# Kernel optimization log

Hardware: AMD Instinct MI355X
Metric: run time of the kernel (lower is better)

Reference implementation:

```python
import jax, jax.numpy as jnp
import numpy as np


def _knn_idx(pts, k):
    # pts: [N, d] -> indices of k nearest neighbors (incl. self, loop=True) [N, k]
    sq = jnp.sum(pts * pts, axis=-1)
    d2 = sq[:, None] + sq[None, :] - 2.0 * (pts @ pts.T)  # [N, N] squared dists
    _, idx = jax.lax.top_k(-d2, k)  # k smallest distances
    return idx


def _graph_conv(x, nbr, Wr, br, Ws):
    # x: [B, N, d_in], nbr: [B, N, k]. GraphConv (aggr='add'):
    # out_i = W_rel @ sum_j x_j + b_rel + W_root @ x_i
    gathered = jax.vmap(lambda xb, ib: xb[ib])(x, nbr)  # [B, N, k, d_in]
    agg = gathered.sum(axis=2)                          # [B, N, d_in]
    return agg @ Wr.T + br + x @ Ws.T


def setup_inputs() -> dict:
    key = jax.random.key(0)
    ks = jax.random.split(key, 10)
    B, N, D, H = 16, 2048, 3, 128
    s = lambda fi, fo: (2.0 / (fi + fo)) ** 0.5
    return {
        "point_cloud": jax.random.normal(ks[0], (B, N, D), dtype=jnp.float32),
        "W1r": jax.random.normal(ks[1], (H, D), dtype=jnp.float32) * s(D, H),
        "b1": jnp.zeros((H,), dtype=jnp.float32),
        "W1s": jax.random.normal(ks[2], (H, D), dtype=jnp.float32) * s(D, H),
        "W2r": jax.random.normal(ks[3], (H, H), dtype=jnp.float32) * s(H, H),
        "b2": jnp.zeros((H,), dtype=jnp.float32),
        "W2s": jax.random.normal(ks[4], (H, H), dtype=jnp.float32) * s(H, H),
        "W3r": jax.random.normal(ks[5], (H, H), dtype=jnp.float32) * s(H, H),
        "b3": jnp.zeros((H,), dtype=jnp.float32),
        "W3s": jax.random.normal(ks[6], (H, H), dtype=jnp.float32) * s(H, H),
        "k": 16,
    }


def reference(point_cloud, W1r, b1, W1s, W2r, b2, W2s, W3r, b3, W3s, k):
    # knn graph per batch element (loop=True: self-loop included, d(i,i)=0)
    nbr = jax.vmap(lambda p: _knn_idx(p, k))(point_cloud)  # [B, N, k]
    x = jax.nn.relu(_graph_conv(point_cloud, nbr, W1r, b1, W1s))
    x = jax.nn.relu(_graph_conv(x, nbr, W2r, b2, W2s))
    x = _graph_conv(x, nbr, W3r, b3, W3s)
    return x  # [B, N, output_dim]
```

## Files before the change

kernel.cpp:

```cpp
#include <hip/hip_runtime.h>
#include <math.h>

#define NPTS 2048
#define BATCH 16
#define KNN 16
#define HID 128
#define RPB 8
#define CAP 128

typedef __attribute__((ext_vector_type(8))) short bf16x8;
typedef __attribute__((ext_vector_type(4))) float f32x4;

__device__ inline unsigned short f2bf(float f) {
    unsigned u = __float_as_uint(f);
    return (unsigned short)((u + 0x7FFFu + ((u >> 16) & 1u)) >> 16);
}
__device__ inline float bflo(unsigned v) { return __uint_as_float(v << 16); }
__device__ inline float bfhi(unsigned v) { return __uint_as_float(v & 0xFFFF0000u); }

__global__ __launch_bounds__(512) void knn_kernel(
    const float* __restrict__ pc, int* __restrict__ nbr,
    const float* __restrict__ W1r, const float* __restrict__ b1,
    const float* __restrict__ W1s, unsigned short* __restrict__ x1)
{
    __shared__ __align__(16) float4 pts[NPTS];
    __shared__ unsigned ckey[RPB][CAP];
    __shared__ unsigned cidx[RPB][CAP];

    const int b = blockIdx.x >> 8;
    const int rblk = blockIdx.x & 255;
    const float* p = pc + (size_t)b * NPTS * 3;

    for (int t = threadIdx.x; t < NPTS; t += 512) {
        float x = p[t * 3 + 0], y = p[t * 3 + 1], z = p[t * 3 + 2];
        pts[t] = make_float4(x, y, z, x * x + y * y + z * z);
    }
    __syncthreads();

    const int w = threadIdx.x >> 6;
    const int lane = threadIdx.x & 63;
    const int i = rblk * RPB + w;
    const float4 pi = pts[i];
    const float piw16 = pi.w + 16.0f;

    unsigned key[32];
    unsigned km = 0xFFFFFFFFu;
    #pragma unroll
    for (int t = 0; t < 32; ++t) {
        float4 c = pts[t * 64 + lane];
        float dot = fmaf(pi.x, c.x, fmaf(pi.y, c.y, pi.z * c.z));
        float d2 = fmaf(-2.0f, dot, piw16 + c.w);
        key[t] = __float_as_uint(d2);
        km = min(km, key[t]);
    }

    unsigned v = km;
    #pragma unroll
    for (int k = 2; k <= 64; k <<= 1) {
        #pragma unroll
        for (int j = k >> 1; j > 0; j >>= 1) {
            unsigned o = (unsigned)__shfl_xor((int)v, j, 64);
            bool sel = ((lane & k) == 0) == ((lane & j) == 0);
            v = sel ? min(v, o) : max(v, o);
        }
    }
    const unsigned T0 = (unsigned)__shfl((int)v, 15, 64);

    unsigned base = 0;
    #pragma unroll 1
    for (int t = 0; t < 32; ++t) {
        bool pred = key[t] <= T0;
        unsigned long long mask = __ballot(pred);
        if (mask) {
            unsigned prefix = __builtin_amdgcn_mbcnt_hi(
                (unsigned)(mask >> 32),
                __builtin_amdgcn_mbcnt_lo((unsigned)mask, 0));
            unsigned pos = base + prefix;
            if (pred && pos < CAP) {
                ckey[w][pos] = key[t];
                cidx[w][pos] = (unsigned)(t * 64 + lane);
            }
            base += (unsigned)__popcll(mask);
        }
    }
    __threadfence_block();
    const int m = (int)base;

    int* out = nbr + ((size_t)b * NPTS + i) * KNN;
    float ax = 0.f, ay = 0.f, az = 0.f;

    if (m <= CAP) {
        unsigned k0 = (lane < m) ? ckey[w][lane] : 0xFFFFFFFFu;
        unsigned k1 = (lane + 64 < m) ? ckey[w][lane + 64] : 0xFFFFFFFFu;
        int r0 = 0, r1 = 0;
        if (m <= 64) {
            #pragma unroll 1
            for (int jj = 0; jj < m; ++jj) {
                unsigned kj = ckey[w][jj];
                r0 += (kj < k0) || (kj == k0 && jj < lane);
            }
        } else {
            #pragma unroll 1
            for (int jj = 0; jj < m; ++jj) {
                unsigned kj = ckey[w][jj];
                r0 += (kj < k0) || (kj == k0 && jj < lane);
                r1 += (kj < k1) || (kj == k1 && jj < lane + 64);
            }
        }
        if (lane < m && r0 < KNN) {
            unsigned j = cidx[w][lane];
            out[r0] = (int)j;
            float4 q = pts[j]; ax += q.x; ay += q.y; az += q.z;
        }
        if (m > 64 && lane + 64 < m && r1 < KNN) {
            unsigned j = cidx[w][lane + 64];
            out[r1] = (int)j;
            float4 q = pts[j]; ax += q.x; ay += q.y; az += q.z;
        }
    } else {
        unsigned T = 0;
        #pragma unroll 1
        for (int bit = 31; bit >= 0; --bit) {
            unsigned trial = T | (1u << bit);
            int cnt = 0;
            #pragma unroll
            for (int t = 0; t < 32; ++t) cnt += (key[t] < trial);
            #pragma unroll
            for (int off = 32; off; off >>= 1)
                cnt += __shfl_xor(cnt, off, 64);
            if (cnt < KNN) T = trial;
        }
        unsigned bs = 0;
        #pragma unroll 1
        for (int t = 0; t < 32; ++t) {
            bool p1 = key[t] < T;
            unsigned long long mask = __ballot(p1);
            if (mask) {
                unsigned prefix = __builtin_amdgcn_mbcnt_hi(
                    (unsigned)(mask >> 32),
                    __builtin_amdgcn_mbcnt_lo((unsigned)mask, 0));
                if (p1) {
                    out[bs + prefix] = t * 64 + lane;
                    float4 q = pts[t * 64 + lane];
                    ax += q.x; ay += q.y; az += q.z;
                }
                bs += (unsigned)__popcll(mask);
            }
        }
        #pragma unroll 1
        for (int t = 0; t < 32 && bs < KNN; ++t) {
            bool p2 = key[t] == T;
            unsigned long long mask = __ballot(p2);
            if (mask) {
                unsigned prefix = __builtin_amdgcn_mbcnt_hi(
                    (unsigned)(mask >> 32),
                    __builtin_amdgcn_mbcnt_lo((unsigned)mask, 0));
                unsigned pos = bs + prefix;
                if (p2 && pos < KNN) {
                    out[pos] = t * 64 + lane;
                    float4 q = pts[t * 64 + lane];
                    ax += q.x; ay += q.y; az += q.z;
                }
                bs += (unsigned)__popcll(mask);
            }
        }
    }

    #pragma unroll
    for (int off = 32; off; off >>= 1) {
        ax += __shfl_xor(ax, off, 64);
        ay += __shfl_xor(ay, off, 64);
        az += __shfl_xor(az, off, 64);
    }

    unsigned short* xrow = x1 + ((size_t)b * NPTS + i) * HID;
    #pragma unroll
    for (int hh = 0; hh < 2; ++hh) {
        int h = lane + hh * 64;
        float acc = b1[h];
        acc += W1r[h * 3 + 0] * ax + W1r[h * 3 + 1] * ay + W1r[h * 3 + 2] * az;
        acc += W1s[h * 3 + 0] * pi.x + W1s[h * 3 + 1] * pi.y + W1s[h * 3 + 2] * pi.z;
        xrow[h] = f2bf(fmaxf(acc, 0.f));
    }
}

__global__ __launch_bounds__(256) void wcvt_kernel(
    const float* __restrict__ a, const float* __restrict__ b,
    const float* __restrict__ c, const float* __restrict__ d,
    unsigned short* __restrict__ out)
{
    int g = blockIdx.x * 256 + threadIdx.x;
    int m = g >> 14;
    const float* s = (m == 0) ? a : (m == 1) ? b : (m == 2) ? c : d;
    out[g] = f2bf(s[g & 16383]);
}

template <bool RELU, bool OUT_BF16>
__global__ __launch_bounds__(512) void conv_fused(
    const unsigned short* __restrict__ x, const int* __restrict__ nbr,
    const unsigned short* __restrict__ Wr, const unsigned short* __restrict__ Ws,
    const float* __restrict__ bias, void* __restrict__ outv)
{
    __shared__ __align__(16) char smem[64 * 132 * 4];
    __shared__ int nbrs[64][17];
    unsigned short (*aggs)[136] = (unsigned short (*)[136])smem;
    float (*outs)[132] = (float (*)[132])smem;

    const int p0 = blockIdx.x * 64;
    const int bt = p0 >> 11;
    const unsigned short* xb = x + ((size_t)bt << 11) * HID;

    for (int e = threadIdx.x; e < 64 * KNN; e += 512)
        nbrs[e >> 4][e & 15] = nbr[(size_t)p0 * KNN + e];
    __syncthreads();

    #pragma unroll
    for (int it = 0; it < 2; ++it) {
        int task = it * 512 + threadIdx.x;
        int c8 = task & 15, pt = task >> 4;
        const unsigned short* base = xb + c8 * 8;
        float s[8] = {0, 0, 0, 0, 0, 0, 0, 0};
        #pragma unroll
        for (int t = 0; t < KNN; ++t) {
            int j = nbrs[pt][t];
            uint4 v = *(const uint4*)(base + (size_t)j * HID);
            s[0] += bflo(v.x); s[1] += bfhi(v.x);
            s[2] += bflo(v.y); s[3] += bfhi(v.y);
            s[4] += bflo(v.z); s[5] += bfhi(v.z);
            s[6] += bflo(v.w); s[7] += bfhi(v.w);
        }
        uint4 ov;
        ov.x = (unsigned)f2bf(s[0]) | ((unsigned)f2bf(s[1]) << 16);
        ov.y = (unsigned)f2bf(s[2]) | ((unsigned)f2bf(s[3]) << 16);
        ov.z = (unsigned)f2bf(s[4]) | ((unsigned)f2bf(s[5]) << 16);
        ov.w = (unsigned)f2bf(s[6]) | ((unsigned)f2bf(s[7]) << 16);
        *(uint4*)&aggs[pt][c8 * 8] = ov;
    }
    __syncthreads();

    const int wv = threadIdx.x >> 6;
    const int lane = threadIdx.x & 63;
    const int ptw = (wv & 1) * 32;
    const int h0w = (wv >> 1) * 32;
    const int row = lane & 15;
    const int quad = lane >> 4;

    f32x4 acc[2][2];
    #pragma unroll
    for (int i = 0; i < 2; ++i)
        #pragma unroll
        for (int n = 0; n < 2; ++n) acc[i][n] = (f32x4){0, 0, 0, 0};

    #pragma unroll
    for (int kc = 0; kc < 4; ++kc) {
        bf16x8 a0 = *(const bf16x8*)&aggs[ptw + row][quad * 8 + kc * 32];
        bf16x8 a1 = *(const bf16x8*)&aggs[ptw + 16 + row][quad * 8 + kc * 32];
        #pragma unroll
        for (int n = 0; n < 2; ++n) {
            bf16x8 bb = *(const bf16x8*)&Wr[(size_t)(h0w + n * 16 + row) * HID
                                            + quad * 8 + kc * 32];
            acc[0][n] = __builtin_amdgcn_mfma_f32_16x16x32_bf16(a0, bb, acc[0][n], 0, 0, 0);
            acc[1][n] = __builtin_amdgcn_mfma_f32_16x16x32_bf16(a1, bb, acc[1][n], 0, 0, 0);
        }
    }
    const unsigned short* xr0 = x + (size_t)(p0 + ptw + row) * HID + quad * 8;
    const unsigned short* xr1 = xr0 + 16 * HID;
    #pragma unroll
    for (int kc = 0; kc < 4; ++kc) {
        bf16x8 a0 = *(const bf16x8*)(xr0 + kc * 32);
        bf16x8 a1 = *(const bf16x8*)(xr1 + kc * 32);
        #pragma unroll
        for (int n = 0; n < 2; ++n) {
            bf16x8 bb = *(const bf16x8*)&Ws[(size_t)(h0w + n * 16 + row) * HID
                                            + quad * 8 + kc * 32];
            acc[0][n] = __builtin_amdgcn_mfma_f32_16x16x32_bf16(a0, bb, acc[0][n], 0, 0, 0);
            acc[1][n] = __builtin_amdgcn_mfma_f32_16x16x32_bf16(a1, bb, acc[1][n], 0, 0, 0);
        }
    }

    __syncthreads();
    #pragma unroll
    for (int n = 0; n < 2; ++n) {
        float bh = bias[h0w + n * 16 + row];
        #pragma unroll
        for (int i = 0; i < 2; ++i) {
            #pragma unroll
            for (int r = 0; r < 4; ++r) {
                int pt = ptw + i * 16 + quad * 4 + r;
                int hh = h0w + n * 16 + row;
                float vv = acc[i][n][r] + bh;
                if (RELU) vv = fmaxf(vv, 0.f);
                if (OUT_BF16) aggs[pt][hh] = f2bf(vv);
                else          outs[pt][hh] = vv;
            }
        }
    }
    __syncthreads();

    if (OUT_BF16) {
        unsigned short* o = (unsigned short*)outv;
        #pragma unroll
        for (int q = 0; q < 2; ++q) {
            int task = q * 512 + threadIdx.x;
            int rr = task >> 4, ch = task & 15;
            *(uint4*)(o + (size_t)(p0 + rr) * HID + ch * 8) =
                *(const uint4*)&aggs[rr][ch * 8];
        }
    } else {
        float* o = (float*)outv;
        #pragma unroll
        for (int q = 0; q < 4; ++q) {
            int task = q * 512 + threadIdx.x;
            int rr = task >> 5, ch = task & 31;
            *(float4*)(o + (size_t)(p0 + rr) * HID + ch * 4) =
                *(const float4*)&outs[rr][ch * 4];
        }
    }
}

extern "C" void kernel_launch(void* const* d_in, const int* in_sizes, int n_in,
                              void* d_out, int out_size, void* d_ws, size_t ws_size,
                              hipStream_t stream)
{
    const float* pc  = (const float*)d_in[0];
    const float* W1r = (const float*)d_in[1];
    const float* b1  = (const float*)d_in[2];
    const float* W1s = (const float*)d_in[3];
    const float* W2r = (const float*)d_in[4];
    const float* b2  = (const float*)d_in[5];
    const float* W2s = (const float*)d_in[6];
    const float* W3r = (const float*)d_in[7];
    const float* b3  = (const float*)d_in[8];
    const float* W3s = (const float*)d_in[9];
    float* out = (float*)d_out;

    char* ws = (char*)d_ws;
    const size_t MB = 1024 * 1024;
    int*            nbr = (int*)ws;
    unsigned short* x1  = (unsigned short*)(ws + 2 * MB);
    unsigned short* x2  = (unsigned short*)(ws + 2 * MB + 8388608);
    unsigned short* wbf = (unsigned short*)(ws + 2 * MB + 2 * 8388608);
    unsigned short* w2r = wbf;
    unsigned short* w2s = wbf + 16384;
    unsigned short* w3r = wbf + 32768;
    unsigned short* w3s = wbf + 49152;

    const int NPOINTS = BATCH * NPTS;

    wcvt_kernel<<<256, 256, 0, stream>>>(W2r, W2s, W3r, W3s, wbf);
    knn_kernel<<<NPOINTS / RPB, 512, 0, stream>>>(pc, nbr, W1r, b1, W1s, x1);

    conv_fused<true, true><<<NPOINTS / 64, 512, 0, stream>>>(
        x1, nbr, w2r, w2s, b2, x2);
    conv_fused<false, false><<<NPOINTS / 64, 512, 0, stream>>>(
        x2, nbr, w3r, w3s, b3, out);
}
```

Baseline: 174.4 us.

## Shrink conv tiles to 16 points, interleave batches across blocks, batch gather loads

The fused graph-conv kernel now processes 16 points per 256-thread block instead of 64 points per 512 threads. Block indices are interleaved across batch elements so concurrently running blocks touch different batches. The neighbor gather issues eight 16-byte loads before accumulating them, which raises memory-level parallelism. Smaller tiles give four times more blocks and less shared memory each, but every block re-reads the full Wr/Ws weight tiles, so weight traffic per point goes up.

```diff
diff --git a/kernel.cpp b/kernel.cpp
--- a/kernel.cpp
+++ b/kernel.cpp
@@ -196,38 +196,43 @@
 }
 
 template <bool RELU, bool OUT_BF16>
-__global__ __launch_bounds__(512) void conv_fused(
+__global__ __launch_bounds__(256) void conv_fused(
     const unsigned short* __restrict__ x, const int* __restrict__ nbr,
     const unsigned short* __restrict__ Wr, const unsigned short* __restrict__ Ws,
     const float* __restrict__ bias, void* __restrict__ outv)
 {
-    __shared__ __align__(16) char smem[64 * 132 * 4];
-    __shared__ int nbrs[64][17];
+    __shared__ __align__(16) char smem[16 * 132 * 4];
+    __shared__ int nbrs[16][17];
     unsigned short (*aggs)[136] = (unsigned short (*)[136])smem;
     float (*outs)[132] = (float (*)[132])smem;
 
-    const int p0 = blockIdx.x * 64;
-    const int bt = p0 >> 11;
+    const int bt = blockIdx.x & 15;
+    const int p0 = bt * NPTS + (blockIdx.x >> 4) * 16;
     const unsigned short* xb = x + ((size_t)bt << 11) * HID;
 
-    for (int e = threadIdx.x; e < 64 * KNN; e += 512)
-        nbrs[e >> 4][e & 15] = nbr[(size_t)p0 * KNN + e];
-    __syncthreads();
-
-    #pragma unroll
-    for (int it = 0; it < 2; ++it) {
-        int task = it * 512 + threadIdx.x;
-        int c8 = task & 15, pt = task >> 4;
+    nbrs[threadIdx.x >> 4][threadIdx.x & 15] =
+        nbr[(size_t)p0 * KNN + threadIdx.x];
+    __syncthreads();
+
+    {
+        const int c8 = threadIdx.x & 15, pt = threadIdx.x >> 4;
         const unsigned short* base = xb + c8 * 8;
         float s[8] = {0, 0, 0, 0, 0, 0, 0, 0};
         #pragma unroll
-        for (int t = 0; t < KNN; ++t) {
-            int j = nbrs[pt][t];
-            uint4 v = *(const uint4*)(base + (size_t)j * HID);
-            s[0] += bflo(v.x); s[1] += bfhi(v.x);
-            s[2] += bflo(v.y); s[3] += bfhi(v.y);
-            s[4] += bflo(v.z); s[5] += bfhi(v.z);
-            s[6] += bflo(v.w); s[7] += bfhi(v.w);
+        for (int half = 0; half < 2; ++half) {
+            uint4 v[8];
+            #pragma unroll
+            for (int t = 0; t < 8; ++t) {
+                int j = nbrs[pt][half * 8 + t];
+                v[t] = *(const uint4*)(base + (size_t)j * HID);
+            }
+            #pragma unroll
+            for (int t = 0; t < 8; ++t) {
+                s[0] += bflo(v[t].x); s[1] += bfhi(v[t].x);
+                s[2] += bflo(v[t].y); s[3] += bfhi(v[t].y);
+                s[4] += bflo(v[t].z); s[5] += bfhi(v[t].z);
+                s[6] += bflo(v[t].w); s[7] += bfhi(v[t].w);
+            }
         }
         uint4 ov;
         ov.x = (unsigned)f2bf(s[0]) | ((unsigned)f2bf(s[1]) << 16);
@@ -240,41 +245,33 @@
 
     const int wv = threadIdx.x >> 6;
     const int lane = threadIdx.x & 63;
-    const int ptw = (wv & 1) * 32;
-    const int h0w = (wv >> 1) * 32;
+    const int h0w = wv * 32;
     const int row = lane & 15;
     const int quad = lane >> 4;
 
-    f32x4 acc[2][2];
-    #pragma unroll
-    for (int i = 0; i < 2; ++i)
-        #pragma unroll
-        for (int n = 0; n < 2; ++n) acc[i][n] = (f32x4){0, 0, 0, 0};
+    f32x4 acc[2];
+    acc[0] = (f32x4){0, 0, 0, 0};
+    acc[1] = (f32x4){0, 0, 0, 0};
 
     #pragma unroll
     for (int kc = 0; kc < 4; ++kc) {
-        bf16x8 a0 = *(const bf16x8*)&aggs[ptw + row][quad * 8 + kc * 32];
-        bf16x8 a1 = *(const bf16x8*)&aggs[ptw + 16 + row][quad * 8 + kc * 32];
+        bf16x8 a0 = *(const bf16x8*)&aggs[row][quad * 8 + kc * 32];
         #pragma unroll
         for (int n = 0; n < 2; ++n) {
             bf16x8 bb = *(const bf16x8*)&Wr[(size_t)(h0w + n * 16 + row) * HID
                                             + quad * 8 + kc * 32];
-            acc[0][n] = __builtin_amdgcn_mfma_f32_16x16x32_bf16(a0, bb, acc[0][n], 0, 0, 0);
-            acc[1][n] = __builtin_amdgcn_mfma_f32_16x16x32_bf16(a1, bb, acc[1][n], 0, 0, 0);
-        }
-    }
-    const unsigned short* xr0 = x + (size_t)(p0 + ptw + row) * HID + quad * 8;
-    const unsigned short* xr1 = xr0 + 16 * HID;
+            acc[n] = __builtin_amdgcn_mfma_f32_16x16x32_bf16(a0, bb, acc[n], 0, 0, 0);
+        }
+    }
+    const unsigned short* xr0 = x + (size_t)(p0 + row) * HID + quad * 8;
     #pragma unroll
     for (int kc = 0; kc < 4; ++kc) {
         bf16x8 a0 = *(const bf16x8*)(xr0 + kc * 32);
-        bf16x8 a1 = *(const bf16x8*)(xr1 + kc * 32);
         #pragma unroll
         for (int n = 0; n < 2; ++n) {
             bf16x8 bb = *(const bf16x8*)&Ws[(size_t)(h0w + n * 16 + row) * HID
                                             + quad * 8 + kc * 32];
-            acc[0][n] = __builtin_amdgcn_mfma_f32_16x16x32_bf16(a0, bb, acc[0][n], 0, 0, 0);
-            acc[1][n] = __builtin_amdgcn_mfma_f32_16x16x32_bf16(a1, bb, acc[1][n], 0, 0, 0);
+            acc[n] = __builtin_amdgcn_mfma_f32_16x16x32_bf16(a0, bb, acc[n], 0, 0, 0);
         }
     }
 
@@ -283,34 +280,27 @@
     for (int n = 0; n < 2; ++n) {
         float bh = bias[h0w + n * 16 + row];
         #pragma unroll
-        for (int i = 0; i < 2; ++i) {
-            #pragma unroll
-            for (int r = 0; r < 4; ++r) {
-                int pt = ptw + i * 16 + quad * 4 + r;
-                int hh = h0w + n * 16 + row;
-                float vv = acc[i][n][r] + bh;
-                if (RELU) vv = fmaxf(vv, 0.f);
-                if (OUT_BF16) aggs[pt][hh] = f2bf(vv);
-                else          outs[pt][hh] = vv;
-            }
+        for (int r = 0; r < 4; ++r) {
+            int pt = quad * 4 + r;
+            int hh = h0w + n * 16 + row;
+            float vv = acc[n][r] + bh;
+            if (RELU) vv = fmaxf(vv, 0.f);
+            if (OUT_BF16) aggs[pt][hh] = f2bf(vv);
+            else          outs[pt][hh] = vv;
         }
     }
     __syncthreads();
 
     if (OUT_BF16) {
         unsigned short* o = (unsigned short*)outv;
-        #pragma unroll
-        for (int q = 0; q < 2; ++q) {
-            int task = q * 512 + threadIdx.x;
-            int rr = task >> 4, ch = task & 15;
-            *(uint4*)(o + (size_t)(p0 + rr) * HID + ch * 8) =
-                *(const uint4*)&aggs[rr][ch * 8];
-        }
+        int rr = threadIdx.x >> 4, ch = threadIdx.x & 15;
+        *(uint4*)(o + (size_t)(p0 + rr) * HID + ch * 8) =
+            *(const uint4*)&aggs[rr][ch * 8];
     } else {
         float* o = (float*)outv;
         #pragma unroll
-        for (int q = 0; q < 4; ++q) {
-            int task = q * 512 + threadIdx.x;
+        for (int q = 0; q < 2; ++q) {
+            int task = q * 256 + threadIdx.x;
             int rr = task >> 5, ch = task & 31;
             *(float4*)(o + (size_t)(p0 + rr) * HID + ch * 4) =
                 *(const float4*)&outs[rr][ch * 4];
@@ -350,8 +340,8 @@
     wcvt_kernel<<<256, 256, 0, stream>>>(W2r, W2s, W3r, W3s, wbf);
     knn_kernel<<<NPOINTS / RPB, 512, 0, stream>>>(pc, nbr, W1r, b1, W1s, x1);
 
-    conv_fused<true, true><<<NPOINTS / 64, 512, 0, stream>>>(
+    conv_fused<true, true><<<NPOINTS / 16, 256, 0, stream>>>(
         x1, nbr, w2r, w2s, b2, x2);
-    conv_fused<false, false><<<NPOINTS / 64, 512, 0, stream>>>(
+    conv_fused<false, false><<<NPOINTS / 16, 256, 0, stream>>>(
         x2, nbr, w3r, w3s, b3, out);
 }
```

After: 182.0 us. +4.4%, slower.

## Chunk activations channel-major and gather neighbors from LDS in separate kernel

Applied to the files above, without the earlier changes.

Activations and weights are stored in a channel-chunked layout of 8 bf16 per point per chunk. Neighbor aggregation moves out of the conv kernel into a new gather kernel. Each gather block loads one 8-channel chunk of a whole batch element (2048 points) into LDS, so the random neighbor reads hit LDS instead of global memory or L2. The matmul kernel then reads the aggregated and root features straight from global memory in the chunked layout. This costs two extra kernel launches and one extra round trip of the aggregate buffer through global memory, and each gather block has only 256 blocks of 1024 threads.

```diff
diff --git a/kernel.cpp b/kernel.cpp
--- a/kernel.cpp
+++ b/kernel.cpp
@@ -5,6 +5,7 @@
 #define BATCH 16
 #define KNN 16
 #define HID 128
+#define NPOINTS (BATCH * NPTS)
 #define RPB 8
 #define CAP 128
 
@@ -18,14 +19,16 @@
 __device__ inline float bflo(unsigned v) { return __uint_as_float(v << 16); }
 __device__ inline float bfhi(unsigned v) { return __uint_as_float(v & 0xFFFF0000u); }
 
+
 __global__ __launch_bounds__(512) void knn_kernel(
     const float* __restrict__ pc, int* __restrict__ nbr,
     const float* __restrict__ W1r, const float* __restrict__ b1,
-    const float* __restrict__ W1s, unsigned short* __restrict__ x1)
+    const float* __restrict__ W1s, unsigned short* __restrict__ x1T)
 {
     __shared__ __align__(16) float4 pts[NPTS];
     __shared__ unsigned ckey[RPB][CAP];
     __shared__ unsigned cidx[RPB][CAP];
+    __shared__ __align__(16) unsigned short xst[RPB][HID];
 
     const int b = blockIdx.x >> 8;
     const int rblk = blockIdx.x & 255;
@@ -173,14 +176,19 @@
         az += __shfl_xor(az, off, 64);
     }
 
-    unsigned short* xrow = x1 + ((size_t)b * NPTS + i) * HID;
     #pragma unroll
     for (int hh = 0; hh < 2; ++hh) {
         int h = lane + hh * 64;
         float acc = b1[h];
         acc += W1r[h * 3 + 0] * ax + W1r[h * 3 + 1] * ay + W1r[h * 3 + 2] * az;
         acc += W1s[h * 3 + 0] * pi.x + W1s[h * 3 + 1] * pi.y + W1s[h * 3 + 2] * pi.z;
-        xrow[h] = f2bf(fmaxf(acc, 0.f));
+        xst[w][h] = f2bf(fmaxf(acc, 0.f));
+    }
+    __syncthreads();
+    if (threadIdx.x < RPB * 16) {
+        int pt = threadIdx.x & 7, cc = threadIdx.x >> 3;
+        uint4 vv = *(const uint4*)&xst[pt][cc * 8];
+        *(uint4*)&x1T[((size_t)cc * NPOINTS + (size_t)b * NPTS + rblk * RPB + pt) * 8] = vv;
     }
 }
 
@@ -191,53 +199,71 @@
 {
     int g = blockIdx.x * 256 + threadIdx.x;
     int m = g >> 14;
+    int e = g & 16383;
+    int r = e >> 7, cch = e & 127;
     const float* s = (m == 0) ? a : (m == 1) ? b : (m == 2) ? c : d;
-    out[g] = f2bf(s[g & 16383]);
-}
-
-template <bool RELU, bool OUT_BF16>
-__global__ __launch_bounds__(512) void conv_fused(
-    const unsigned short* __restrict__ x, const int* __restrict__ nbr,
-    const unsigned short* __restrict__ Wr, const unsigned short* __restrict__ Ws,
-    const float* __restrict__ bias, void* __restrict__ outv)
-{
-    __shared__ __align__(16) char smem[64 * 132 * 4];
-    __shared__ int nbrs[64][17];
-    unsigned short (*aggs)[136] = (unsigned short (*)[136])smem;
-    float (*outs)[132] = (float (*)[132])smem;
-
-    const int p0 = blockIdx.x * 64;
-    const int bt = p0 >> 11;
-    const unsigned short* xb = x + ((size_t)bt << 11) * HID;
-
-    for (int e = threadIdx.x; e < 64 * KNN; e += 512)
-        nbrs[e >> 4][e & 15] = nbr[(size_t)p0 * KNN + e];
+    out[m * 16384 + ((cch >> 3) * 128 + r) * 8 + (cch & 7)] = f2bf(s[e]);
+}
+
+__global__ __launch_bounds__(1024) void gather_kernel(
+    const unsigned short* __restrict__ xT, const int* __restrict__ nbr,
+    unsigned short* __restrict__ aggT)
+{
+    __shared__ __align__(16) unsigned short rows[NPTS * 12];
+    const int b = blockIdx.x & 15;
+    const int cc = blockIdx.x >> 4;
+    const unsigned short* src = xT + ((size_t)cc * NPOINTS + (size_t)b * NPTS) * 8;
+
+    #pragma unroll
+    for (int rr = 0; rr < 2; ++rr) {
+        int t = rr * 1024 + threadIdx.x;
+        uint4 vv = *(const uint4*)(src + t * 8);
+        *(uint2*)&rows[t * 12] = make_uint2(vv.x, vv.y);
+        *(uint2*)&rows[t * 12 + 4] = make_uint2(vv.z, vv.w);
+    }
     __syncthreads();
 
-    #pragma unroll
-    for (int it = 0; it < 2; ++it) {
-        int task = it * 512 + threadIdx.x;
-        int c8 = task & 15, pt = task >> 4;
-        const unsigned short* base = xb + c8 * 8;
+    const int* nb = nbr + (size_t)b * NPTS * KNN;
+    unsigned short* dst = aggT + ((size_t)cc * NPOINTS + (size_t)b * NPTS) * 8;
+
+    #pragma unroll
+    for (int rr = 0; rr < 2; ++rr) {
+        int pt = rr * 1024 + threadIdx.x;
+        const int4* nr4 = (const int4*)(nb + (size_t)pt * KNN);
+        int4 n0 = nr4[0], n1 = nr4[1], n2 = nr4[2], n3 = nr4[3];
+        int idx[16] = {n0.x, n0.y, n0.z, n0.w, n1.x, n1.y, n1.z, n1.w,
+                       n2.x, n2.y, n2.z, n2.w, n3.x, n3.y, n3.z, n3.w};
         float s[8] = {0, 0, 0, 0, 0, 0, 0, 0};
         #pragma unroll
         for (int t = 0; t < KNN; ++t) {
-            int j = nbrs[pt][t];
-            uint4 v = *(const uint4*)(base + (size_t)j * HID);
-            s[0] += bflo(v.x); s[1] += bfhi(v.x);
-            s[2] += bflo(v.y); s[3] += bfhi(v.y);
-            s[4] += bflo(v.z); s[5] += bfhi(v.z);
-            s[6] += bflo(v.w); s[7] += bfhi(v.w);
+            int j = idx[t];
+            uint2 va = *(const uint2*)&rows[j * 12];
+            uint2 vb = *(const uint2*)&rows[j * 12 + 4];
+            s[0] += bflo(va.x); s[1] += bfhi(va.x);
+            s[2] += bflo(va.y); s[3] += bfhi(va.y);
+            s[4] += bflo(vb.x); s[5] += bfhi(vb.x);
+            s[6] += bflo(vb.y); s[7] += bfhi(vb.y);
         }
         uint4 ov;
         ov.x = (unsigned)f2bf(s[0]) | ((unsigned)f2bf(s[1]) << 16);
         ov.y = (unsigned)f2bf(s[2]) | ((unsigned)f2bf(s[3]) << 16);
         ov.z = (unsigned)f2bf(s[4]) | ((unsigned)f2bf(s[5]) << 16);
         ov.w = (unsigned)f2bf(s[6]) | ((unsigned)f2bf(s[7]) << 16);
-        *(uint4*)&aggs[pt][c8 * 8] = ov;
-    }
-    __syncthreads();
-
+        *(uint4*)(dst + (size_t)pt * 8) = ov;
+    }
+}
+
+template <bool RELU, bool OUT_CHUNKED>
+__global__ __launch_bounds__(512) void convmm_kernel(
+    const unsigned short* __restrict__ aggT, const unsigned short* __restrict__ xT,
+    const unsigned short* __restrict__ wTr, const unsigned short* __restrict__ wTs,
+    const float* __restrict__ bias, void* __restrict__ outv)
+{
+    __shared__ __align__(16) char smem[64 * 132 * 4];
+    unsigned short (*obf)[136] = (unsigned short (*)[136])smem;
+    float (*of32)[132] = (float (*)[132])smem;
+
+    const int p0 = blockIdx.x * 64;
     const int wv = threadIdx.x >> 6;
     const int lane = threadIdx.x & 63;
     const int ptw = (wv & 1) * 32;
@@ -253,32 +279,29 @@
 
     #pragma unroll
     for (int kc = 0; kc < 4; ++kc) {
-        bf16x8 a0 = *(const bf16x8*)&aggs[ptw + row][quad * 8 + kc * 32];
-        bf16x8 a1 = *(const bf16x8*)&aggs[ptw + 16 + row][quad * 8 + kc * 32];
+        const int pl = quad + 4 * kc;
+        bf16x8 a0 = *(const bf16x8*)(aggT + ((size_t)pl * NPOINTS + p0 + ptw + row) * 8);
+        bf16x8 a1 = *(const bf16x8*)(aggT + ((size_t)pl * NPOINTS + p0 + ptw + 16 + row) * 8);
         #pragma unroll
         for (int n = 0; n < 2; ++n) {
-            bf16x8 bb = *(const bf16x8*)&Wr[(size_t)(h0w + n * 16 + row) * HID
-                                            + quad * 8 + kc * 32];
+            bf16x8 bb = *(const bf16x8*)(wTr + ((size_t)pl * HID + h0w + n * 16 + row) * 8);
             acc[0][n] = __builtin_amdgcn_mfma_f32_16x16x32_bf16(a0, bb, acc[0][n], 0, 0, 0);
             acc[1][n] = __builtin_amdgcn_mfma_f32_16x16x32_bf16(a1, bb, acc[1][n], 0, 0, 0);
         }
     }
-    const unsigned short* xr0 = x + (size_t)(p0 + ptw + row) * HID + quad * 8;
-    const unsigned short* xr1 = xr0 + 16 * HID;
     #pragma unroll
     for (int kc = 0; kc < 4; ++kc) {
-        bf16x8 a0 = *(const bf16x8*)(xr0 + kc * 32);
-        bf16x8 a1 = *(const bf16x8*)(xr1 + kc * 32);
+        const int pl = quad + 4 * kc;
+        bf16x8 a0 = *(const bf16x8*)(xT + ((size_t)pl * NPOINTS + p0 + ptw + row) * 8);
+        bf16x8 a1 = *(const bf16x8*)(xT + ((size_t)pl * NPOINTS + p0 + ptw + 16 + row) * 8);
         #pragma unroll
         for (int n = 0; n < 2; ++n) {
-            bf16x8 bb = *(const bf16x8*)&Ws[(size_t)(h0w + n * 16 + row) * HID
-                                            + quad * 8 + kc * 32];
+            bf16x8 bb = *(const bf16x8*)(wTs + ((size_t)pl * HID + h0w + n * 16 + row) * 8);
             acc[0][n] = __builtin_amdgcn_mfma_f32_16x16x32_bf16(a0, bb, acc[0][n], 0, 0, 0);
             acc[1][n] = __builtin_amdgcn_mfma_f32_16x16x32_bf16(a1, bb, acc[1][n], 0, 0, 0);
         }
     }
 
-    __syncthreads();
     #pragma unroll
     for (int n = 0; n < 2; ++n) {
         float bh = bias[h0w + n * 16 + row];
@@ -290,21 +313,21 @@
                 int hh = h0w + n * 16 + row;
                 float vv = acc[i][n][r] + bh;
                 if (RELU) vv = fmaxf(vv, 0.f);
-                if (OUT_BF16) aggs[pt][hh] = f2bf(vv);
-                else          outs[pt][hh] = vv;
+                if (OUT_CHUNKED) obf[pt][hh] = f2bf(vv);
+                else             of32[pt][hh] = vv;
             }
         }
     }
     __syncthreads();
 
-    if (OUT_BF16) {
+    if (OUT_CHUNKED) {
         unsigned short* o = (unsigned short*)outv;
         #pragma unroll
         for (int q = 0; q < 2; ++q) {
             int task = q * 512 + threadIdx.x;
-            int rr = task >> 4, ch = task & 15;
-            *(uint4*)(o + (size_t)(p0 + rr) * HID + ch * 8) =
-                *(const uint4*)&aggs[rr][ch * 8];
+            int pt = task & 63, cc = task >> 6;
+            *(uint4*)(o + ((size_t)cc * NPOINTS + p0 + pt) * 8) =
+                *(const uint4*)&obf[pt][cc * 8];
         }
     } else {
         float* o = (float*)outv;
@@ -313,7 +336,7 @@
             int task = q * 512 + threadIdx.x;
             int rr = task >> 5, ch = task & 31;
             *(float4*)(o + (size_t)(p0 + rr) * HID + ch * 4) =
-                *(const float4*)&outs[rr][ch * 4];
+                *(const float4*)&of32[rr][ch * 4];
         }
     }
 }
@@ -336,22 +359,25 @@
 
     char* ws = (char*)d_ws;
     const size_t MB = 1024 * 1024;
-    int*            nbr = (int*)ws;
-    unsigned short* x1  = (unsigned short*)(ws + 2 * MB);
-    unsigned short* x2  = (unsigned short*)(ws + 2 * MB + 8388608);
-    unsigned short* wbf = (unsigned short*)(ws + 2 * MB + 2 * 8388608);
-    unsigned short* w2r = wbf;
-    unsigned short* w2s = wbf + 16384;
-    unsigned short* w3r = wbf + 32768;
-    unsigned short* w3s = wbf + 49152;
-
-    const int NPOINTS = BATCH * NPTS;
-
-    wcvt_kernel<<<256, 256, 0, stream>>>(W2r, W2s, W3r, W3s, wbf);
-    knn_kernel<<<NPOINTS / RPB, 512, 0, stream>>>(pc, nbr, W1r, b1, W1s, x1);
-
-    conv_fused<true, true><<<NPOINTS / 64, 512, 0, stream>>>(
-        x1, nbr, w2r, w2s, b2, x2);
-    conv_fused<false, false><<<NPOINTS / 64, 512, 0, stream>>>(
-        x2, nbr, w3r, w3s, b3, out);
-}
+    const size_t XSZ = (size_t)NPOINTS * HID * 2;
+    int*            nbr  = (int*)ws;
+    unsigned short* x1T  = (unsigned short*)(ws + 2 * MB);
+    unsigned short* x2T  = (unsigned short*)(ws + 2 * MB + XSZ);
+    unsigned short* aggT = (unsigned short*)(ws + 2 * MB + 2 * XSZ);
+    unsigned short* wT   = (unsigned short*)(ws + 2 * MB + 3 * XSZ);
+    unsigned short* w2rT = wT;
+    unsigned short* w2sT = wT + 16384;
+    unsigned short* w3rT = wT + 32768;
+    unsigned short* w3sT = wT + 49152;
+
+    wcvt_kernel<<<256, 256, 0, stream>>>(W2r, W2s, W3r, W3s, wT);
+    knn_kernel<<<NPOINTS / RPB, 512, 0, stream>>>(pc, nbr, W1r, b1, W1s, x1T);
+
+    gather_kernel<<<256, 1024, 0, stream>>>(x1T, nbr, aggT);
+    convmm_kernel<true, true><<<NPOINTS / 64, 512, 0, stream>>>(
+        aggT, x1T, w2rT, w2sT, b2, x2T);
+
+    gather_kernel<<<256, 1024, 0, stream>>>(x2T, nbr, aggT);
+    convmm_kernel<false, false><<<NPOINTS / 64, 512, 0, stream>>>(
+        aggT, x2T, w3rT, w3sT, b3, out);
+}
```

Result: faster. 168.5 us (-3.4%).
